# Performance work log

Measured on AMD Instinct MI355X. Metric: run time of the kernel, lower is better.

Reference implementation:

```python
import jax, jax.numpy as jnp
import numpy as np
from jax import lax

DN = ('NCHW', 'OIHW', 'NCHW')
EPS = 1e-5


def _conv3x3(x, w, b):
    return lax.conv_general_dilated(x, w, (1, 1), 'SAME', dimension_numbers=DN) + b[:, None, None]


def _conv1x1(x, w, b):
    return jnp.einsum('bchw,oc->bohw', x, w) + b[:, None, None]


def _dwconv3x3(x, w, b):
    # w: (C,1,3,3), depthwise
    C = x.shape[1]
    return lax.conv_general_dilated(x, w, (1, 1), 'SAME', feature_group_count=C,
                                    dimension_numbers=DN) + b[:, None, None]


def setup_inputs() -> dict:
    key = jax.random.key(0)
    ks = jax.random.split(key, 24)
    b, t, c, h, w = 2, 8, 64, 160, 160
    r, K = c // 4, 3

    def n(k, shape, s=0.05):
        return jax.random.normal(k, shape, dtype=jnp.float32) * s

    return {
        'feature': n(ks[0], (b, t, c, h, w), 1.0),
        'kc_w1': n(ks[1], (r, c)),
        'kc_bn_gamma': jnp.ones((r,), jnp.float32),
        'kc_bn_beta': jnp.zeros((r,), jnp.float32),
        'kc_bn_mean': jnp.zeros((r,), jnp.float32),
        'kc_bn_var': jnp.ones((r,), jnp.float32),
        'kc_w2': n(ks[2], (c * K * K, r)),
        'kc_b2': n(ks[3], (c * K * K,)),
        'kc_bias': n(ks[4], (c,)),
        'conv1_w': n(ks[5], (2 * c, 2 * c, 3, 3)),
        'conv1_b': n(ks[6], (2 * c,)),
        'pi1_w': n(ks[7], (4 * c, c)),
        'pi1_b': n(ks[8], (4 * c,)),
        'dw1_w': n(ks[9], (4 * c, 1, 3, 3)),
        'dw1_b': n(ks[10], (4 * c,)),
        'po1_w': n(ks[11], (c, 4 * c)),
        'po1_b': n(ks[12], (c,)),
        'pi2_w': n(ks[13], (4 * c, c)),
        'pi2_b': n(ks[14], (4 * c,)),
        'dw2_w': n(ks[15], (4 * c, 1, 3, 3)),
        'dw2_b': n(ks[16], (4 * c,)),
        'po2_w': n(ks[17], (c, 4 * c)),
        'po2_b': n(ks[18], (c,)),
    }


def reference(feature, kc_w1, kc_bn_gamma, kc_bn_beta, kc_bn_mean, kc_bn_var,
              kc_w2, kc_b2, kc_bias, conv1_w, conv1_b,
              pi1_w, pi1_b, dw1_w, dw1_b, po1_w, po1_b,
              pi2_w, pi2_b, dw2_w, dw2_b, po2_w, po2_b):
    b, t, c, h, w = feature.shape
    K = int(round((kc_w2.shape[0] // c) ** 0.5))  # dynamic kernel size (3)

    def dyn_dwconv(x_feat, y):
        # kernel generation: GAP -> 1x1 -> BN(eval) -> ReLU -> 1x1
        pool = x_feat.mean(axis=(2, 3))                           # (b, c)
        z = pool @ kc_w1.T                                        # (b, r)
        z = (z - kc_bn_mean) * jax.lax.rsqrt(kc_bn_var + EPS) * kc_bn_gamma + kc_bn_beta
        z = jax.nn.relu(z)
        wd = (z @ kc_w2.T + kc_b2).reshape(b, c, K, K)            # per-sample dw kernels

        def per_sample(yi, wi):
            return lax.conv_general_dilated(yi[None], wi[:, None], (1, 1), 'SAME',
                                            feature_group_count=c,
                                            dimension_numbers=DN)[0]
        out = jax.vmap(per_sample)(y, wd)                         # (b, c, h, w)
        return out + kc_bias[None, :, None, None]

    def step(feat_prop, x_feat):
        fp = dyn_dwconv(x_feat, feat_prop)
        fusion = jnp.concatenate([x_feat, fp], axis=1)
        fusion = jax.nn.leaky_relu(_conv3x3(fusion, conv1_w, conv1_b), 0.1)
        f1, f2 = fusion[:, :c], fusion[:, c:]
        g1 = jax.nn.sigmoid(_conv1x1(_dwconv3x3(_conv1x1(f1, pi1_w, pi1_b), dw1_w, dw1_b), po1_w, po1_b))
        g2 = jax.nn.sigmoid(_conv1x1(_dwconv3x3(_conv1x1(f2, pi2_w, pi2_b), dw2_w, dw2_b), po2_w, po2_b))
        new_fp = f1 * g1 + f2 * g2
        return new_fp, new_fp

    init = feature[:, t - 1]                                      # frame t-1
    xs = jnp.moveaxis(jnp.flip(feature[:, :t - 1], axis=1), 1, 0)  # frames t-2 .. 0
    _, ys = lax.scan(step, init, xs)                              # (t-1, b, c, h, w)
    full = jnp.concatenate([jnp.flip(ys, axis=0), init[None]], axis=0)
    return jnp.moveaxis(full, 0, 1)                               # (b, t, c, h, w)
```

## Files before the change

kernel.cpp:

```cpp
#include <hip/hip_runtime.h>

typedef __attribute__((ext_vector_type(8))) __bf16 bf16x8;
typedef __attribute__((ext_vector_type(4))) float f32x4;

#define BB 2
#define TT 8
#define CC 64
#define HH 160
#define WW 160
#define HWW 25600
#define RR 16
#define C2 128
#define C4 256
#define C8 512
#define NSTEP 7
#define CHW (CC*HWW)
#define EPSV 1e-5f

__device__ __forceinline__ f32x4 mfma16(bf16x8 a, bf16x8 b, f32x4 c) {
    return __builtin_amdgcn_mfma_f32_16x16x32_bf16(a, b, c, 0, 0, 0);
}

__global__ void pool_kernel(const float* __restrict__ feat, float* __restrict__ pool) {
    int idx = blockIdx.x;
    int b = idx / (NSTEP * CC);
    int f = (idx / CC) % NSTEP;
    int c = idx % CC;
    const float4* src = (const float4*)(feat + ((size_t)(b * TT + f) * CC + c) * HWW);
    float s = 0.f;
    for (int i = threadIdx.x; i < HWW / 4; i += 256) {
        float4 v = src[i];
        s += v.x + v.y + v.z + v.w;
    }
    __shared__ float sm[256];
    sm[threadIdx.x] = s;
    __syncthreads();
    for (int off = 128; off > 0; off >>= 1) {
        if (threadIdx.x < off) sm[threadIdx.x] += sm[threadIdx.x + off];
        __syncthreads();
    }
    if (threadIdx.x == 0) pool[idx] = sm[0] * (1.0f / HWW);
}

__global__ void wd_kernel(const float* __restrict__ pool, const float* __restrict__ w1,
                          const float* __restrict__ gamma, const float* __restrict__ beta,
                          const float* __restrict__ mean, const float* __restrict__ var,
                          const float* __restrict__ w2, const float* __restrict__ b2,
                          float* __restrict__ wdT) {
    int bf = blockIdx.x;
    __shared__ float z[RR];
    int tid = threadIdx.x;
    if (tid < RR) {
        const float* p = pool + bf * CC;
        float s = 0.f;
        for (int c = 0; c < CC; c++) s += p[c] * w1[tid * CC + c];
        s = (s - mean[tid]) * rsqrtf(var[tid] + EPSV) * gamma[tid] + beta[tid];
        z[tid] = s > 0.f ? s : 0.f;
    }
    __syncthreads();
    for (int o = tid; o < CC * 9; o += 64) {
        float s = b2[o];
        #pragma unroll
        for (int r = 0; r < RR; r++) s += z[r] * w2[o * RR + r];
        int c = o / 9, t = o % 9;
        wdT[bf * 576 + t * CC + c] = s;
    }
}

__global__ void copy_init_kernel(const float* __restrict__ feat, float* __restrict__ out) {
    int i = blockIdx.x * 256 + threadIdx.x;
    int n4 = CHW / 4;
    int b = i / n4;
    int r = i % n4;
    size_t off = ((size_t)(b * TT + (TT - 1)) * CHW) / 4 + r;
    ((float4*)out)[off] = ((const float4*)feat)[off];
}

__global__ void prep_weights(const float* __restrict__ c1w,
                             const float* __restrict__ pi1, const float* __restrict__ pi2,
                             const float* __restrict__ po1, const float* __restrict__ po2,
                             const float* __restrict__ dw1, const float* __restrict__ dw2,
                             const float* __restrict__ dw1b, const float* __restrict__ dw2b,
                             __bf16* __restrict__ Bc1,
                             __bf16* __restrict__ Bpi1, __bf16* __restrict__ Bpi2,
                             __bf16* __restrict__ Bpo1, __bf16* __restrict__ Bpo2,
                             float* __restrict__ dwT12, float* __restrict__ dwb12,
                             __bf16* __restrict__ Bpk) {
    int idx = blockIdx.x * 256 + threadIdx.x;
    if (idx < 147456) {
        int oc = idx / 1152, k = idx % 1152;
        int t = k >> 7, ic = k & 127;
        Bc1[idx] = (__bf16)c1w[(oc * 128 + ic) * 9 + t];
        return;
    }
    idx -= 147456;
    if (idx < 16384) { Bpi1[idx] = (__bf16)pi1[idx]; return; }
    idx -= 16384;
    if (idx < 16384) { Bpi2[idx] = (__bf16)pi2[idx]; return; }
    idx -= 16384;
    if (idx < 16384) { Bpo1[idx] = (__bf16)po1[idx]; return; }
    idx -= 16384;
    if (idx < 16384) { Bpo2[idx] = (__bf16)po2[idx]; return; }
    idx -= 16384;
    if (idx < 4608) {
        int t = idx / 512, c = idx % 512;
        dwT12[t * C8 + c] = (c < 256) ? dw1[c * 9 + t] : dw2[(c - 256) * 9 + t];
        return;
    }
    idx -= 4608;
    if (idx < 512) { dwb12[idx] = (idx < 256) ? dw1b[idx] : dw2b[idx - 256]; return; }
    idx -= 512;
    if (idx < 32768) {
        int j = idx & 7, ln = (idx >> 3) & 63, nt = (idx >> 9) & 3, kg = (idx >> 11) & 3, cc = idx >> 13;
        int lmx = ln & 15, lqx = ln >> 4;
        int oc = nt * 16 + lmx;
        int ci = (cc & 1) * 128 + kg * 32 + lqx * 8 + j;
        const float* src = (cc >> 1) ? po2 : po1;
        Bpk[idx] = (__bf16)src[oc * C4 + ci];
    }
}

__global__ void featPM_kernel(const float* __restrict__ feat, __bf16* __restrict__ featPM) {
    __shared__ float Lt[64 * 68];
    int bf = blockIdx.x / 400;
    int p0 = (blockIdx.x % 400) * 64;
    int tid = threadIdx.x;
    int c = tid & 63, half = tid >> 6;
    const float* src = feat + ((size_t)bf * CC + c) * HWW + p0 + half * 16;
    #pragma unroll
    for (int k = 0; k < 16; k++) Lt[(half * 16 + k) * 68 + c] = src[k];
    __syncthreads();
    int cg = tid & 7;
    #pragma unroll
    for (int pass = 0; pass < 2; pass++) {
        int pl = (tid >> 3) + pass * 32;
        bf16x8 o;
        #pragma unroll
        for (int j = 0; j < 8; j++) o[j] = (__bf16)Lt[pl * 68 + cg * 8 + j];
        *(bf16x8*)(featPM + ((size_t)bf * HWW + p0 + pl) * CC + cg * 8) = o;
    }
}

__global__ void dyndw_kernel(const __bf16* __restrict__ src, size_t bstr,
                             const float* __restrict__ wdT, const float* __restrict__ kc_bias,
                             __bf16* __restrict__ fpPM, int fx) {
    int gi = blockIdx.x * 256 + threadIdx.x;
    int c0 = (gi & 7) * 8;
    int rem = gi >> 3;
    int p = rem % HWW;
    int bb = rem / HWW;
    int py = p / WW, px = p % WW;
    float acc[8];
    float4 k0 = *(const float4*)(kc_bias + c0);
    float4 k1 = *(const float4*)(kc_bias + c0 + 4);
    acc[0]=k0.x; acc[1]=k0.y; acc[2]=k0.z; acc[3]=k0.w;
    acc[4]=k1.x; acc[5]=k1.y; acc[6]=k1.z; acc[7]=k1.w;
    const float* wb = wdT + (size_t)(bb * NSTEP + fx) * 576;
    const __bf16* sb = src + (size_t)bb * bstr;
    const int dyA[9] = {-1,-1,-1,0,0,0,1,1,1};
    const int dxA[9] = {-1,0,1,-1,0,1,-1,0,1};
    #pragma unroll
    for (int t = 0; t < 9; t++) {
        int dy = dyA[t], dx = dxA[t];
        if ((unsigned)(py + dy) < HH && (unsigned)(px + dx) < WW) {
            bf16x8 uv = *(const bf16x8*)(sb + (size_t)(p + dy * WW + dx) * CC + c0);
            float4 w0 = *(const float4*)(wb + t * CC + c0);
            float4 w1 = *(const float4*)(wb + t * CC + c0 + 4);
            acc[0] += (float)uv[0] * w0.x; acc[1] += (float)uv[1] * w0.y;
            acc[2] += (float)uv[2] * w0.z; acc[3] += (float)uv[3] * w0.w;
            acc[4] += (float)uv[4] * w1.x; acc[5] += (float)uv[5] * w1.y;
            acc[6] += (float)uv[6] * w1.z; acc[7] += (float)uv[7] * w1.w;
        }
    }
    bf16x8 o;
    #pragma unroll
    for (int j = 0; j < 8; j++) o[j] = (__bf16)acc[j];
    *(bf16x8*)(fpPM + ((size_t)bb * HWW + p) * CC + c0) = o;
}

__global__ void conv1_gemm(const __bf16* __restrict__ featPM, const __bf16* __restrict__ fpPM,
                           const __bf16* __restrict__ Bc1, const float* __restrict__ bias,
                           __bf16* __restrict__ fusionPM, int fx) {
    __shared__ __align__(16) __bf16 As[128 * 40];
    __shared__ __align__(16) __bf16 Bs[128 * 40];
    const int tid = threadIdx.x;
    const int bb = blockIdx.x / 200;
    const int p0 = (blockIdx.x % 200) * 128;
    const int i = tid >> 1, h = tid & 1;
    const int p = p0 + i;
    const int py = p / WW, px = p % WW;
    const __bf16* featB = featPM + (size_t)(bb * TT + fx) * HWW * CC;
    const __bf16* fpB   = fpPM + (size_t)bb * HWW * CC;
    const int wv = tid >> 6, lane = tid & 63, lm = lane & 15, lq = lane >> 4;
    f32x4 acc[2][8];
    #pragma unroll
    for (int mt = 0; mt < 2; mt++)
        #pragma unroll
        for (int nt = 0; nt < 8; nt++) acc[mt][nt] = (f32x4){0.f, 0.f, 0.f, 0.f};

    for (int ks = 0; ks < 36; ks++) {
        const int t = ks >> 2, ci0 = (ks & 3) * 32;
        const int dy = t / 3 - 1, dx = t % 3 - 1;
        const bool valid = ((unsigned)(py + dy) < HH) && ((unsigned)(px + dx) < WW);
        uint4 a0 = {0,0,0,0}, a1 = {0,0,0,0};
        if (valid) {
            const __bf16* sp = (ci0 < 64)
                ? featB + (size_t)(p + dy * WW + dx) * CC + ci0
                : fpB   + (size_t)(p + dy * WW + dx) * CC + (ci0 - 64);
            a0 = *(const uint4*)(sp + h * 16);
            a1 = *(const uint4*)(sp + h * 16 + 8);
        }
        const __bf16* bp = Bc1 + (size_t)i * 1152 + ks * 32 + h * 16;
        uint4 w0q = *(const uint4*)(bp);
        uint4 w1q = *(const uint4*)(bp + 8);
        __syncthreads();
        *(uint4*)&As[i * 40 + h * 16]     = a0;
        *(uint4*)&As[i * 40 + h * 16 + 8] = a1;
        *(uint4*)&Bs[i * 40 + h * 16]     = w0q;
        *(uint4*)&Bs[i * 40 + h * 16 + 8] = w1q;
        __syncthreads();
        bf16x8 af0 = *(const bf16x8*)&As[((wv * 2 + 0) * 16 + lm) * 40 + lq * 8];
        bf16x8 af1 = *(const bf16x8*)&As[((wv * 2 + 1) * 16 + lm) * 40 + lq * 8];
        #pragma unroll
        for (int nt = 0; nt < 8; nt++) {
            bf16x8 bf = *(const bf16x8*)&Bs[(nt * 16 + lm) * 40 + lq * 8];
            acc[0][nt] = mfma16(af0, bf, acc[0][nt]);
            acc[1][nt] = mfma16(af1, bf, acc[1][nt]);
        }
    }
    __bf16* ob = fusionPM + (size_t)bb * HWW * C2;
    #pragma unroll
    for (int mt = 0; mt < 2; mt++) {
        #pragma unroll
        for (int nt = 0; nt < 8; nt++) {
            const int oc = nt * 16 + lm;
            const float bs = bias[oc];
            #pragma unroll
            for (int r = 0; r < 4; r++) {
                const int pp = p0 + (wv * 2 + mt) * 16 + lq * 4 + r;
                float v = acc[mt][nt][r] + bs;
                v = v > 0.f ? v : 0.1f * v;
                ob[(size_t)pp * C2 + oc] = (__bf16)v;
            }
        }
    }
}

__global__ void pw1_gemm(const __bf16* __restrict__ fusionPM,
                         const __bf16* __restrict__ Bpi1, const __bf16* __restrict__ Bpi2,
                         const float* __restrict__ pi1b, const float* __restrict__ pi2b,
                         __bf16* __restrict__ u12PM) {
    __shared__ __align__(16) __bf16 As[128 * 40];
    __shared__ __align__(16) __bf16 Bs[128 * 40];
    const int tid = threadIdx.x;
    const int bb = blockIdx.x / 800;
    const int rem = blockIdx.x % 800;
    const int p0 = (rem >> 2) * 128;
    const int nb = rem & 3;
    const int br = nb >> 1, ns = nb & 1;
    const __bf16* Bpi = br ? Bpi2 : Bpi1;
    const float* bias = br ? pi2b : pi1b;
    const int i = tid >> 1, h = tid & 1;
    const int p = p0 + i;
    const __bf16* fB = fusionPM + (size_t)bb * HWW * C2 + br * CC;
    const int wv = tid >> 6, lane = tid & 63, lm = lane & 15, lq = lane >> 4;
    f32x4 acc[2][8];
    #pragma unroll
    for (int mt = 0; mt < 2; mt++)
        #pragma unroll
        for (int nt = 0; nt < 8; nt++) acc[mt][nt] = (f32x4){0.f, 0.f, 0.f, 0.f};

    #pragma unroll
    for (int ks = 0; ks < 2; ks++) {
        const int ci0 = ks * 32;
        const __bf16* sp = fB + (size_t)p * C2 + ci0 + h * 16;
        uint4 a0 = *(const uint4*)(sp);
        uint4 a1 = *(const uint4*)(sp + 8);
        const __bf16* bp = Bpi + (size_t)(ns * 128 + i) * 64 + ci0 + h * 16;
        uint4 w0q = *(const uint4*)(bp);
        uint4 w1q = *(const uint4*)(bp + 8);
        __syncthreads();
        *(uint4*)&As[i * 40 + h * 16]     = a0;
        *(uint4*)&As[i * 40 + h * 16 + 8] = a1;
        *(uint4*)&Bs[i * 40 + h * 16]     = w0q;
        *(uint4*)&Bs[i * 40 + h * 16 + 8] = w1q;
        __syncthreads();
        bf16x8 af0 = *(const bf16x8*)&As[((wv * 2 + 0) * 16 + lm) * 40 + lq * 8];
        bf16x8 af1 = *(const bf16x8*)&As[((wv * 2 + 1) * 16 + lm) * 40 + lq * 8];
        #pragma unroll
        for (int nt = 0; nt < 8; nt++) {
            bf16x8 bf = *(const bf16x8*)&Bs[(nt * 16 + lm) * 40 + lq * 8];
            acc[0][nt] = mfma16(af0, bf, acc[0][nt]);
            acc[1][nt] = mfma16(af1, bf, acc[1][nt]);
        }
    }
    __bf16* ub = u12PM + (size_t)bb * HWW * C8;
    #pragma unroll
    for (int mt = 0; mt < 2; mt++) {
        #pragma unroll
        for (int nt = 0; nt < 8; nt++) {
            const int ocl = ns * 128 + nt * 16 + lm;
            const int oc = br * 256 + ocl;
            const float bs = bias[ocl];
            #pragma unroll
            for (int r = 0; r < 4; r++) {
                const int pp = p0 + (wv * 2 + mt) * 16 + lq * 4 + r;
                ub[(size_t)pp * C8 + oc] = (__bf16)(acc[mt][nt][r] + bs);
            }
        }
    }
}

__global__ void dwpw2_gemm(const __bf16* __restrict__ u12PM,
                           const float* __restrict__ dwT12, const float* __restrict__ dwb12,
                           const __bf16* __restrict__ Bpk,
                           const float* __restrict__ pob1, const float* __restrict__ pob2,
                           const __bf16* __restrict__ fusionPM,
                           float* __restrict__ out, __bf16* __restrict__ outPM, int fx) {
    __shared__ __align__(16) __bf16 Vt[32 * 136];
    const int tid = threadIdx.x;
    const int bid = blockIdx.x;
    const int wg = (bid & 7) * 200 + (bid >> 3);
    const int bb = wg / 800;
    const int p0 = (wg % 800) * 32;
    const __bf16* uB = u12PM + (size_t)bb * HWW * C8;
    const int wv = tid >> 6, lane = tid & 63, lm = lane & 15, lq = lane >> 4;
    const int mt = wv & 1, nh = wv >> 1;
    const int cg = tid & 15, prow = tid >> 4;
    const int pA = p0 + prow;
    const int py = pA / WW;
    const int px0 = pA % WW;

    f32x4 acc[2][2];
    #pragma unroll
    for (int b = 0; b < 2; b++)
        #pragma unroll
        for (int n = 0; n < 2; n++) acc[b][n] = (f32x4){0.f, 0.f, 0.f, 0.f};

    #pragma unroll
    for (int cc = 0; cc < 4; cc++) {
        const int c0 = cc * 128 + cg * 8;
        float4 b0 = *(const float4*)(dwb12 + c0);
        float4 b1 = *(const float4*)(dwb12 + c0 + 4);
        float accv[2][8];
        accv[0][0]=b0.x; accv[0][1]=b0.y; accv[0][2]=b0.z; accv[0][3]=b0.w;
        accv[0][4]=b1.x; accv[0][5]=b1.y; accv[0][6]=b1.z; accv[0][7]=b1.w;
        #pragma unroll
        for (int j = 0; j < 8; j++) accv[1][j] = accv[0][j];
        #pragma unroll
        for (int t = 0; t < 9; t++) {
            const int dy = t / 3 - 1, dx = t % 3 - 1;
            const bool vy = (unsigned)(py + dy) < HH;
            float4 w0 = *(const float4*)(dwT12 + t * C8 + c0);
            float4 w1 = *(const float4*)(dwT12 + t * C8 + c0 + 4);
            float wr[8] = {w0.x, w0.y, w0.z, w0.w, w1.x, w1.y, w1.z, w1.w};
            if (vy && (unsigned)(px0 + dx) < WW) {
                bf16x8 uv = *(const bf16x8*)(uB + (size_t)(pA + dy * WW + dx) * C8 + c0);
                #pragma unroll
                for (int j = 0; j < 8; j++) accv[0][j] += (float)uv[j] * wr[j];
            }
            if (vy && (unsigned)(px0 + 16 + dx) < WW) {
                bf16x8 uv = *(const bf16x8*)(uB + (size_t)(pA + 16 + dy * WW + dx) * C8 + c0);
                #pragma unroll
                for (int j = 0; j < 8; j++) accv[1][j] += (float)uv[j] * wr[j];
            }
        }
        bf16x8 o0, o1;
        #pragma unroll
        for (int j = 0; j < 8; j++) { o0[j] = (__bf16)accv[0][j]; o1[j] = (__bf16)accv[1][j]; }
        __syncthreads();
        *(bf16x8*)&Vt[prow * 136 + cg * 8]        = o0;
        *(bf16x8*)&Vt[(16 + prow) * 136 + cg * 8] = o1;
        __syncthreads();
        const int br = cc >> 1;
        const __bf16* bbase = Bpk + cc * 8192 + (size_t)lane * 8;
        #pragma unroll
        for (int kg = 0; kg < 4; kg++) {
            bf16x8 af = *(const bf16x8*)&Vt[(mt * 16 + lm) * 136 + kg * 32 + lq * 8];
            #pragma unroll
            for (int ntl = 0; ntl < 2; ntl++) {
                bf16x8 bfr = *(const bf16x8*)(bbase + kg * 2048 + (nh * 2 + ntl) * 512);
                acc[br][ntl] = mfma16(af, bfr, acc[br][ntl]);
            }
        }
    }
    const __bf16* fB = fusionPM + (size_t)bb * HWW * C2;
    __bf16* opB = outPM + (size_t)bb * HWW * CC;
    float* outp = out + (size_t)(bb * TT + fx) * CC * HWW;
    const int ppb = p0 + mt * 16 + lq * 4;
    #pragma unroll
    for (int ntl = 0; ntl < 2; ntl++) {
        const int oc = (nh * 2 + ntl) * 16 + lm;
        const float bs1 = pob1[oc];
        const float bs2 = pob2[oc];
        float4 vo;
        #pragma unroll
        for (int r = 0; r < 4; r++) {
            const int pp = ppb + r;
            float g1 = 1.f / (1.f + __expf(-(acc[0][ntl][r] + bs1)));
            float g2 = 1.f / (1.f + __expf(-(acc[1][ntl][r] + bs2)));
            float f1 = (float)fB[(size_t)pp * C2 + oc];
            float f2 = (float)fB[(size_t)pp * C2 + CC + oc];
            float val = f1 * g1 + f2 * g2;
            (&vo.x)[r] = val;
            opB[(size_t)pp * CC + oc] = (__bf16)val;
        }
        *(float4*)(outp + (size_t)oc * HWW + ppb) = vo;
    }
}

extern "C" void kernel_launch(void* const* d_in, const int* in_sizes, int n_in,
                              void* d_out, int out_size, void* d_ws, size_t ws_size,
                              hipStream_t stream) {
    const float* feat     = (const float*)d_in[0];
    const float* kc_w1    = (const float*)d_in[1];
    const float* kc_g     = (const float*)d_in[2];
    const float* kc_be    = (const float*)d_in[3];
    const float* kc_mu    = (const float*)d_in[4];
    const float* kc_var   = (const float*)d_in[5];
    const float* kc_w2    = (const float*)d_in[6];
    const float* kc_b2    = (const float*)d_in[7];
    const float* kc_bias  = (const float*)d_in[8];
    const float* conv1_w  = (const float*)d_in[9];
    const float* conv1_b  = (const float*)d_in[10];
    const float* pi1_w    = (const float*)d_in[11];
    const float* pi1_b    = (const float*)d_in[12];
    const float* dw1_w    = (const float*)d_in[13];
    const float* dw1_b    = (const float*)d_in[14];
    const float* po1_w    = (const float*)d_in[15];
    const float* po1_b    = (const float*)d_in[16];
    const float* pi2_w    = (const float*)d_in[17];
    const float* pi2_b    = (const float*)d_in[18];
    const float* dw2_w    = (const float*)d_in[19];
    const float* dw2_b    = (const float*)d_in[20];
    const float* po2_w    = (const float*)d_in[21];
    const float* po2_b    = (const float*)d_in[22];
    float* out = (float*)d_out;

    char* W = (char*)d_ws;
    __bf16* featPM   = (__bf16*)W; W += (size_t)BB * TT * HWW * CC * 2;
    __bf16* fpPM     = (__bf16*)W; W += (size_t)BB * HWW * CC * 2;
    __bf16* fusionPM = (__bf16*)W; W += (size_t)BB * HWW * C2 * 2;
    __bf16* u12PM    = (__bf16*)W; W += (size_t)BB * HWW * C8 * 2;
    __bf16* outPM    = (__bf16*)W; W += (size_t)BB * HWW * CC * 2;
    __bf16* Bc1      = (__bf16*)W; W += 294912;
    __bf16* Bpi1     = (__bf16*)W; W += 32768;
    __bf16* Bpi2     = (__bf16*)W; W += 32768;
    __bf16* Bpo1     = (__bf16*)W; W += 32768;
    __bf16* Bpo2     = (__bf16*)W; W += 32768;
    __bf16* Bpk      = (__bf16*)W; W += 65536;
    float*  dwT12    = (float*)W;  W += 18432;
    float*  dwb12    = (float*)W;  W += 2048;
    float*  poolb    = (float*)W;  W += 4096;
    float*  wdT      = (float*)W;  W += 32256;

    prep_weights<<<980, 256, 0, stream>>>(conv1_w, pi1_w, pi2_w, po1_w, po2_w, dw1_w, dw2_w,
                                          dw1_b, dw2_b,
                                          Bc1, Bpi1, Bpi2, Bpo1, Bpo2, dwT12, dwb12, Bpk);
    featPM_kernel<<<BB * TT * 400, 256, 0, stream>>>(feat, featPM);
    pool_kernel<<<BB * NSTEP * CC, 256, 0, stream>>>(feat, poolb);
    wd_kernel<<<BB * NSTEP, 64, 0, stream>>>(poolb, kc_w1, kc_g, kc_be, kc_mu, kc_var, kc_w2, kc_b2, wdT);
    copy_init_kernel<<<BB * CHW / 4 / 256, 256, 0, stream>>>(feat, out);

    for (int i = 0; i < NSTEP; i++) {
        int fx = NSTEP - 1 - i;
        const __bf16* src = (fx == NSTEP - 1) ? (featPM + (size_t)(TT - 1) * HWW * CC) : outPM;
        size_t bstr = (fx == NSTEP - 1) ? (size_t)TT * HWW * CC : (size_t)HWW * CC;
        dyndw_kernel<<<BB * HWW * 8 / 256, 256, 0, stream>>>(src, bstr, wdT, kc_bias, fpPM, fx);
        conv1_gemm<<<BB * 200, 256, 0, stream>>>(featPM, fpPM, Bc1, conv1_b, fusionPM, fx);
        pw1_gemm<<<BB * 800, 256, 0, stream>>>(fusionPM, Bpi1, Bpi2, pi1_b, pi2_b, u12PM);
        dwpw2_gemm<<<BB * 800, 256, 0, stream>>>(u12PM, dwT12, dwb12, Bpk, po1_b, po2_b, fusionPM, out, outPM, fx);
    }
}
```

Before: 1.089 ms.

## Shrink conv1 tiles for more blocks and stage depthwise halo in LDS

conv1_gemm now uses 32-pixel tiles with 128 threads and 1600 blocks per batch pair instead of 128-pixel tiles with 256 threads. The 400 blocks of the old grid underfilled the GPU, and the smaller tiles spread the work over more CUs. dwpw2_gemm now stages a 3x34-pixel halo of the u12 tile into shared memory once per channel chunk, so the nine taps read LDS instead of issuing repeated global loads. It also unpacks bf16 pairs with bit shifts and uses packed 2-wide FMAs. The costs are a 4x larger weight reload in conv1, since every block streams the full weight matrix, and extra LDS use and barriers in dwpw2.

Result: slower. 1.228 ms (+12.7%).

```diff
diff --git a/kernel.cpp b/kernel.cpp
--- a/kernel.cpp
+++ b/kernel.cpp
@@ -2,6 +2,7 @@
 
 typedef __attribute__((ext_vector_type(8))) __bf16 bf16x8;
 typedef __attribute__((ext_vector_type(4))) float f32x4;
+typedef __attribute__((ext_vector_type(2))) float f32x2;
 
 #define BB 2
 #define TT 8
@@ -19,6 +20,13 @@
 
 __device__ __forceinline__ f32x4 mfma16(bf16x8 a, bf16x8 b, f32x4 c) {
     return __builtin_amdgcn_mfma_f32_16x16x32_bf16(a, b, c, 0, 0, 0);
+}
+
+__device__ __forceinline__ void bpk_fma(unsigned d, f32x2 w, f32x2& a) {
+    f32x2 u;
+    u.x = __uint_as_float(d << 16);
+    u.y = __uint_as_float(d & 0xffff0000u);
+    a = __builtin_elementwise_fma(u, w, a);
 }
 
 __global__ void pool_kernel(const float* __restrict__ feat, float* __restrict__ pool) {
@@ -181,67 +189,64 @@
 __global__ void conv1_gemm(const __bf16* __restrict__ featPM, const __bf16* __restrict__ fpPM,
                            const __bf16* __restrict__ Bc1, const float* __restrict__ bias,
                            __bf16* __restrict__ fusionPM, int fx) {
-    __shared__ __align__(16) __bf16 As[128 * 40];
+    __shared__ __align__(16) __bf16 As[32 * 40];
     __shared__ __align__(16) __bf16 Bs[128 * 40];
     const int tid = threadIdx.x;
-    const int bb = blockIdx.x / 200;
-    const int p0 = (blockIdx.x % 200) * 128;
-    const int i = tid >> 1, h = tid & 1;
-    const int p = p0 + i;
+    const int bid = blockIdx.x;
+    const int wg = (bid & 7) * 200 + (bid >> 3);
+    const int bb = wg / 800;
+    const int p0 = (wg % 800) * 32;
+    const int ar = tid >> 2, ah = tid & 3;
+    const int p = p0 + ar;
     const int py = p / WW, px = p % WW;
     const __bf16* featB = featPM + (size_t)(bb * TT + fx) * HWW * CC;
     const __bf16* fpB   = fpPM + (size_t)bb * HWW * CC;
     const int wv = tid >> 6, lane = tid & 63, lm = lane & 15, lq = lane >> 4;
-    f32x4 acc[2][8];
-    #pragma unroll
-    for (int mt = 0; mt < 2; mt++)
-        #pragma unroll
-        for (int nt = 0; nt < 8; nt++) acc[mt][nt] = (f32x4){0.f, 0.f, 0.f, 0.f};
+    f32x4 acc[8];
+    #pragma unroll
+    for (int nt = 0; nt < 8; nt++) acc[nt] = (f32x4){0.f, 0.f, 0.f, 0.f};
 
     for (int ks = 0; ks < 36; ks++) {
         const int t = ks >> 2, ci0 = (ks & 3) * 32;
         const int dy = t / 3 - 1, dx = t % 3 - 1;
         const bool valid = ((unsigned)(py + dy) < HH) && ((unsigned)(px + dx) < WW);
-        uint4 a0 = {0,0,0,0}, a1 = {0,0,0,0};
+        uint4 a0 = {0,0,0,0};
         if (valid) {
             const __bf16* sp = (ci0 < 64)
                 ? featB + (size_t)(p + dy * WW + dx) * CC + ci0
                 : fpB   + (size_t)(p + dy * WW + dx) * CC + (ci0 - 64);
-            a0 = *(const uint4*)(sp + h * 16);
-            a1 = *(const uint4*)(sp + h * 16 + 8);
-        }
-        const __bf16* bp = Bc1 + (size_t)i * 1152 + ks * 32 + h * 16;
-        uint4 w0q = *(const uint4*)(bp);
-        uint4 w1q = *(const uint4*)(bp + 8);
-        __syncthreads();
-        *(uint4*)&As[i * 40 + h * 16]     = a0;
-        *(uint4*)&As[i * 40 + h * 16 + 8] = a1;
-        *(uint4*)&Bs[i * 40 + h * 16]     = w0q;
-        *(uint4*)&Bs[i * 40 + h * 16 + 8] = w1q;
-        __syncthreads();
-        bf16x8 af0 = *(const bf16x8*)&As[((wv * 2 + 0) * 16 + lm) * 40 + lq * 8];
-        bf16x8 af1 = *(const bf16x8*)&As[((wv * 2 + 1) * 16 + lm) * 40 + lq * 8];
+            a0 = *(const uint4*)(sp + ah * 8);
+        }
+        const __bf16* bp = Bc1 + (size_t)tid * 1152 + ks * 32;
+        uint4 w0 = *(const uint4*)(bp);
+        uint4 w1 = *(const uint4*)(bp + 8);
+        uint4 w2 = *(const uint4*)(bp + 16);
+        uint4 w3 = *(const uint4*)(bp + 24);
+        __syncthreads();
+        *(uint4*)&As[ar * 40 + ah * 8] = a0;
+        *(uint4*)&Bs[tid * 40 + 0]  = w0;
+        *(uint4*)&Bs[tid * 40 + 8]  = w1;
+        *(uint4*)&Bs[tid * 40 + 16] = w2;
+        *(uint4*)&Bs[tid * 40 + 24] = w3;
+        __syncthreads();
+        bf16x8 af = *(const bf16x8*)&As[(wv * 16 + lm) * 40 + lq * 8];
         #pragma unroll
         for (int nt = 0; nt < 8; nt++) {
-            bf16x8 bf = *(const bf16x8*)&Bs[(nt * 16 + lm) * 40 + lq * 8];
-            acc[0][nt] = mfma16(af0, bf, acc[0][nt]);
-            acc[1][nt] = mfma16(af1, bf, acc[1][nt]);
+            bf16x8 bfr = *(const bf16x8*)&Bs[(nt * 16 + lm) * 40 + lq * 8];
+            acc[nt] = mfma16(af, bfr, acc[nt]);
         }
     }
     __bf16* ob = fusionPM + (size_t)bb * HWW * C2;
     #pragma unroll
-    for (int mt = 0; mt < 2; mt++) {
-        #pragma unroll
-        for (int nt = 0; nt < 8; nt++) {
-            const int oc = nt * 16 + lm;
-            const float bs = bias[oc];
-            #pragma unroll
-            for (int r = 0; r < 4; r++) {
-                const int pp = p0 + (wv * 2 + mt) * 16 + lq * 4 + r;
-                float v = acc[mt][nt][r] + bs;
-                v = v > 0.f ? v : 0.1f * v;
-                ob[(size_t)pp * C2 + oc] = (__bf16)v;
-            }
+    for (int nt = 0; nt < 8; nt++) {
+        const int oc = nt * 16 + lm;
+        const float bs = bias[oc];
+        #pragma unroll
+        for (int r = 0; r < 4; r++) {
+            const int pp = p0 + wv * 16 + lq * 4 + r;
+            float v = acc[nt][r] + bs;
+            v = v > 0.f ? v : 0.1f * v;
+            ob[(size_t)pp * C2 + oc] = (__bf16)v;
         }
     }
 }
@@ -317,19 +322,18 @@
                            const float* __restrict__ pob1, const float* __restrict__ pob2,
                            const __bf16* __restrict__ fusionPM,
                            float* __restrict__ out, __bf16* __restrict__ outPM, int fx) {
+    __shared__ __align__(16) __bf16 uL[3 * 34 * 128];
     __shared__ __align__(16) __bf16 Vt[32 * 136];
     const int tid = threadIdx.x;
     const int bid = blockIdx.x;
     const int wg = (bid & 7) * 200 + (bid >> 3);
     const int bb = wg / 800;
     const int p0 = (wg % 800) * 32;
+    const int py = p0 / WW, px0 = p0 % WW;
     const __bf16* uB = u12PM + (size_t)bb * HWW * C8;
     const int wv = tid >> 6, lane = tid & 63, lm = lane & 15, lq = lane >> 4;
     const int mt = wv & 1, nh = wv >> 1;
     const int cg = tid & 15, prow = tid >> 4;
-    const int pA = p0 + prow;
-    const int py = pA / WW;
-    const int px0 = pA % WW;
 
     f32x4 acc[2][2];
     #pragma unroll
@@ -337,41 +341,61 @@
         #pragma unroll
         for (int n = 0; n < 2; n++) acc[b][n] = (f32x4){0.f, 0.f, 0.f, 0.f};
 
+    const int rbase = py - 1, cbase = px0 - 1;
+
     #pragma unroll
     for (int cc = 0; cc < 4; cc++) {
-        const int c0 = cc * 128 + cg * 8;
-        float4 b0 = *(const float4*)(dwb12 + c0);
-        float4 b1 = *(const float4*)(dwb12 + c0 + 4);
-        float accv[2][8];
-        accv[0][0]=b0.x; accv[0][1]=b0.y; accv[0][2]=b0.z; accv[0][3]=b0.w;
-        accv[0][4]=b1.x; accv[0][5]=b1.y; accv[0][6]=b1.z; accv[0][7]=b1.w;
-        #pragma unroll
-        for (int j = 0; j < 8; j++) accv[1][j] = accv[0][j];
+        const int c0ch = cc * 128;
+        #pragma unroll
+        for (int it = 0; it < 7; it++) {
+            int idx = it * 256 + tid;
+            if (idx < 1632) {
+                int s = idx >> 4, part = idx & 15;
+                int r = s / 34, c = s - r * 34;
+                int gr = rbase + r, gc = cbase + c;
+                uint4 v = {0,0,0,0};
+                if ((unsigned)gr < HH && (unsigned)gc < WW)
+                    v = *(const uint4*)(uB + (size_t)(gr * WW + gc) * C8 + c0ch + part * 8);
+                *(uint4*)&uL[idx * 8] = v;
+            }
+        }
+        __syncthreads();
+
+        const int c0 = c0ch + cg * 8;
+        f32x2 a0[4], a1[4];
+        {
+            float4 b0 = *(const float4*)(dwb12 + c0);
+            float4 b1 = *(const float4*)(dwb12 + c0 + 4);
+            a0[0] = (f32x2){b0.x, b0.y}; a0[1] = (f32x2){b0.z, b0.w};
+            a0[2] = (f32x2){b1.x, b1.y}; a0[3] = (f32x2){b1.z, b1.w};
+            #pragma unroll
+            for (int k = 0; k < 4; k++) a1[k] = a0[k];
+        }
         #pragma unroll
         for (int t = 0; t < 9; t++) {
             const int dy = t / 3 - 1, dx = t % 3 - 1;
-            const bool vy = (unsigned)(py + dy) < HH;
             float4 w0 = *(const float4*)(dwT12 + t * C8 + c0);
             float4 w1 = *(const float4*)(dwT12 + t * C8 + c0 + 4);
-            float wr[8] = {w0.x, w0.y, w0.z, w0.w, w1.x, w1.y, w1.z, w1.w};
-            if (vy && (unsigned)(px0 + dx) < WW) {
-                bf16x8 uv = *(const bf16x8*)(uB + (size_t)(pA + dy * WW + dx) * C8 + c0);
-                #pragma unroll
-                for (int j = 0; j < 8; j++) accv[0][j] += (float)uv[j] * wr[j];
-            }
-            if (vy && (unsigned)(px0 + 16 + dx) < WW) {
-                bf16x8 uv = *(const bf16x8*)(uB + (size_t)(pA + 16 + dy * WW + dx) * C8 + c0);
-                #pragma unroll
-                for (int j = 0; j < 8; j++) accv[1][j] += (float)uv[j] * wr[j];
-            }
+            f32x2 wp[4] = {(f32x2){w0.x, w0.y}, (f32x2){w0.z, w0.w},
+                           (f32x2){w1.x, w1.y}, (f32x2){w1.z, w1.w}};
+            const int base = ((1 + dy) * 34 + 1 + dx) * 128 + cg * 8;
+            uint4 ua = *(const uint4*)&uL[base + prow * 128];
+            uint4 ub4 = *(const uint4*)&uL[base + (prow + 16) * 128];
+            bpk_fma(ua.x, wp[0], a0[0]); bpk_fma(ua.y, wp[1], a0[1]);
+            bpk_fma(ua.z, wp[2], a0[2]); bpk_fma(ua.w, wp[3], a0[3]);
+            bpk_fma(ub4.x, wp[0], a1[0]); bpk_fma(ub4.y, wp[1], a1[1]);
+            bpk_fma(ub4.z, wp[2], a1[2]); bpk_fma(ub4.w, wp[3], a1[3]);
         }
         bf16x8 o0, o1;
         #pragma unroll
-        for (int j = 0; j < 8; j++) { o0[j] = (__bf16)accv[0][j]; o1[j] = (__bf16)accv[1][j]; }
-        __syncthreads();
+        for (int k = 0; k < 4; k++) {
+            o0[2 * k] = (__bf16)a0[k].x; o0[2 * k + 1] = (__bf16)a0[k].y;
+            o1[2 * k] = (__bf16)a1[k].x; o1[2 * k + 1] = (__bf16)a1[k].y;
+        }
         *(bf16x8*)&Vt[prow * 136 + cg * 8]        = o0;
         *(bf16x8*)&Vt[(16 + prow) * 136 + cg * 8] = o1;
         __syncthreads();
+
         const int br = cc >> 1;
         const __bf16* bbase = Bpk + cc * 8192 + (size_t)lane * 8;
         #pragma unroll
@@ -467,7 +491,7 @@
         const __bf16* src = (fx == NSTEP - 1) ? (featPM + (size_t)(TT - 1) * HWW * CC) : outPM;
         size_t bstr = (fx == NSTEP - 1) ? (size_t)TT * HWW * CC : (size_t)HWW * CC;
         dyndw_kernel<<<BB * HWW * 8 / 256, 256, 0, stream>>>(src, bstr, wdT, kc_bias, fpPM, fx);
-        conv1_gemm<<<BB * 200, 256, 0, stream>>>(featPM, fpPM, Bc1, conv1_b, fusionPM, fx);
+        conv1_gemm<<<BB * 800, 128, 0, stream>>>(featPM, fpPM, Bc1, conv1_b, fusionPM, fx);
         pw1_gemm<<<BB * 800, 256, 0, stream>>>(fusionPM, Bpi1, Bpi2, pi1_b, pi2_b, u12PM);
         dwpw2_gemm<<<BB * 800, 256, 0, stream>>>(u12PM, dwT12, dwb12, Bpk, po1_b, po2_b, fusionPM, out, outPM, fx);
     }
```
